# Kernel tuning notes

Hardware: AMD Instinct MI355X
Metric: run time of the kernel (lower is better)

The kernel has to match this reference:

```python
import jax, jax.numpy as jnp
import numpy as np

D_MODEL = 1024
N_HEADS = 16
D_HEAD = 64


def setup_inputs() -> dict:
    key = jax.random.key(0)
    ks = jax.random.split(key, 9)
    B, T = 2, 2048
    s_in = 1.0 / np.sqrt(D_MODEL)
    s_o = 1.0 / np.sqrt(N_HEADS * D_HEAD)
    return {
        "x": jax.random.normal(ks[0], (B, T, D_MODEL), dtype=jnp.float32),
        "wq": jax.random.normal(ks[1], (D_MODEL, N_HEADS * D_HEAD), dtype=jnp.float32) * s_in,
        "bq": jax.random.normal(ks[2], (N_HEADS * D_HEAD,), dtype=jnp.float32) * 0.01,
        "wk": jax.random.normal(ks[3], (D_MODEL, N_HEADS * D_HEAD), dtype=jnp.float32) * s_in,
        "bk": jax.random.normal(ks[4], (N_HEADS * D_HEAD,), dtype=jnp.float32) * 0.01,
        "wv": jax.random.normal(ks[5], (D_MODEL, N_HEADS * D_HEAD), dtype=jnp.float32) * s_in,
        "bv": jax.random.normal(ks[6], (N_HEADS * D_HEAD,), dtype=jnp.float32) * 0.01,
        "wo": jax.random.normal(ks[7], (N_HEADS * D_HEAD, D_MODEL), dtype=jnp.float32) * s_o,
        "bo": jax.random.normal(ks[8], (D_MODEL,), dtype=jnp.float32) * 0.01,
    }


def reference(x, wq, bq, wk, bk, wv, bv, wo, bo):
    B, T, _ = x.shape
    H, Dh = N_HEADS, D_HEAD
    # projections -> [B, H, T, Dh]
    q = (x @ wq + bq).reshape(B, T, H, Dh).transpose(0, 2, 1, 3)
    k = (x @ wk + bk).reshape(B, T, H, Dh).transpose(0, 2, 1, 3)
    v = (x @ wv + bv).reshape(B, T, H, Dh).transpose(0, 2, 1, 3)
    scale = 1.0 / np.sqrt(Dh).astype(np.float32)
    attn = jnp.einsum("bhqd,bhkd->bhqk", q, k) * scale  # [B,H,T,T]
    causal = jnp.tril(jnp.ones((T, T), dtype=bool))
    attn = jnp.where(causal, attn, jnp.float32(-jnp.inf))
    attn = jax.nn.softmax(attn, axis=-1)
    out = jnp.einsum("bhqk,bhkd->bhqd", attn, v)  # [B,H,T,Dh]
    out = out.transpose(0, 2, 1, 3).reshape(B, T, H * Dh)
    return out @ wo + bo
```

## Files before the change

### kernel.cpp

```cpp
#include <hip/hip_runtime.h>
#include <math.h>

#define D_MODEL 1024
#define N_HEADS 16
#define D_HEAD  64
#define B_SZ    2
#define T_SEQ   2048

typedef short bf16x8 __attribute__((ext_vector_type(8)));
typedef short bf16x4 __attribute__((ext_vector_type(4)));
typedef float f32x4  __attribute__((ext_vector_type(4)));
typedef unsigned short us4 __attribute__((ext_vector_type(4)));

__device__ __forceinline__ unsigned short f2bf(float f) {
  union { float f; unsigned u; } v; v.f = f;
  unsigned r = v.u + 0x7FFFu + ((v.u >> 16) & 1u);
  return (unsigned short)(r >> 16);
}
__device__ __forceinline__ float bf2f(unsigned short s) {
  union { unsigned u; float f; } v; v.u = ((unsigned)s) << 16;
  return v.f;
}
__device__ __forceinline__ unsigned pack2_rtz(float lo, float hi) {
  union { float f; unsigned u; } a, b; a.f = hi; b.f = lo;
  return __builtin_amdgcn_perm(a.u, b.u, 0x07060302u);
}

__device__ __forceinline__ void async_copy16(const unsigned short* g, unsigned short* l) {
  __builtin_amdgcn_global_load_lds(
      (__attribute__((address_space(1))) void*)(g),
      (__attribute__((address_space(3))) void*)(l), 16, 0, 0);
}

__device__ __forceinline__ unsigned short* opart_ptr(
    unsigned short* wtd, unsigned short* xbd, int p) {
  const size_t off = (size_t)p * 2048;
  const size_t RA  = (size_t)3 * 1024 * 1024;
  return (off < RA) ? (wtd + off) : (xbd + (off - RA));
}

__global__ __launch_bounds__(256) void conv_all(
    const float* __restrict__ x,
    const float* __restrict__ wq, const float* __restrict__ wk,
    const float* __restrict__ wv, const float* __restrict__ wo,
    unsigned short* __restrict__ wt, unsigned short* __restrict__ xb)
{
  const int z = blockIdx.z;
  if (z < 4) {
    const float* W = (z == 0) ? wq : (z == 1) ? wk : (z == 2) ? wv : wo;
    unsigned short* O = wt + (size_t)z * D_MODEL * D_MODEL;
    __shared__ float t[32][33];
    const int tx = threadIdx.x & 31, ty = threadIdx.x >> 5;
    const int kb = blockIdx.x * 32, nb = blockIdx.y * 32;
    #pragma unroll
    for (int i = 0; i < 4; i++)
      t[ty + i * 8][tx] = W[(size_t)(kb + ty + i * 8) * D_MODEL + nb + tx];
    __syncthreads();
    #pragma unroll
    for (int i = 0; i < 4; i++)
      O[(size_t)(nb + ty + i * 8) * D_MODEL + kb + tx] = f2bf(t[tx][ty + i * 8]);
  } else {
    const int row = (z - 4) * 1024 + blockIdx.y * 32 + (threadIdx.x >> 3);
    const int col = blockIdx.x * 32 + (threadIdx.x & 7) * 4;
    float4 v = *(const float4*)&x[(size_t)row * D_MODEL + col];
    us4 o = { f2bf(v.x), f2bf(v.y), f2bf(v.z), f2bf(v.w) };
    *(us4*)&xb[(size_t)row * D_MODEL + col] = o;
  }
}

#define BKg 64
#define QSCALE 0.180336879f

__global__ __launch_bounds__(256) void qkv_gemm(
    const unsigned short* __restrict__ A, const unsigned short* __restrict__ Bt,
    const float* __restrict__ bq, const float* __restrict__ bk,
    const float* __restrict__ bv, unsigned short* __restrict__ qkv,
    unsigned short* __restrict__ vT)
{
  __shared__ unsigned short As[128 * BKg];
  __shared__ unsigned short Bs[64 * BKg];

  const int tid  = threadIdx.x;
  const int wv   = tid >> 6;
  const int lane = tid & 63;
  const int lr   = lane & 15;
  const int quad = lane >> 4;
  const int wm   = wv >> 1;
  const int wn   = wv & 1;
  const int row0 = blockIdx.x * 128;
  const int col0 = blockIdx.y * 64;
  const int K = D_MODEL;

  const int mid = col0 >> 10;
  const float* bias = (mid == 0) ? bq : (mid == 1) ? bk : bv;

  f32x4 acc[8];
  #pragma unroll
  for (int i = 0; i < 8; i++) acc[i] = (f32x4){0.f, 0.f, 0.f, 0.f};

  for (int k0 = 0; k0 < K; k0 += BKg) {
    #pragma unroll
    for (int it = 0; it < 4; it++) {
      const int gg = wv * 256 + it * 64 + lane;
      const int r  = gg >> 3;
      const int gc = ((gg & 7) ^ (r & 7)) * 8;
      async_copy16(A + (size_t)(row0 + r) * K + k0 + gc,
                   (unsigned short*)As + (size_t)(wv * 256 + it * 64) * 8);
    }
    #pragma unroll
    for (int it = 0; it < 2; it++) {
      const int gg = wv * 128 + it * 64 + lane;
      const int r  = gg >> 3;
      const int gc = ((gg & 7) ^ (r & 7)) * 8;
      async_copy16(Bt + (size_t)(col0 + r) * K + k0 + gc,
                   (unsigned short*)Bs + (size_t)(wv * 128 + it * 64) * 8);
    }
    __syncthreads();

    if (mid == 2) {
      bf16x8 aF[4][2], bF[2][2];
      #pragma unroll
      for (int hf = 0; hf < 2; hf++) {
        const int kc = (hf * 4 + quad) ^ (lr & 7);
        #pragma unroll
        for (int mi = 0; mi < 4; mi++)
          aF[mi][hf] = *(const bf16x8*)&As[(wm * 64 + mi * 16 + lr) * BKg + kc * 8];
        #pragma unroll
        for (int ni = 0; ni < 2; ni++)
          bF[ni][hf] = *(const bf16x8*)&Bs[(wn * 32 + ni * 16 + lr) * BKg + kc * 8];
      }
      #pragma unroll
      for (int hf = 0; hf < 2; hf++)
        #pragma unroll
        for (int mi = 0; mi < 4; mi++)
          #pragma unroll
          for (int ni = 0; ni < 2; ni++)
            acc[mi * 2 + ni] = __builtin_amdgcn_mfma_f32_16x16x32_bf16(
                aF[mi][hf], bF[ni][hf], acc[mi * 2 + ni], 0, 0, 0);
    } else {
      bf16x8 aF[2][2], bF[4][2];
      #pragma unroll
      for (int hf = 0; hf < 2; hf++) {
        const int kc = (hf * 4 + quad) ^ (lr & 7);
        #pragma unroll
        for (int mi = 0; mi < 2; mi++)
          aF[mi][hf] = *(const bf16x8*)&Bs[(wm * 32 + mi * 16 + lr) * BKg + kc * 8];
        #pragma unroll
        for (int ni = 0; ni < 4; ni++)
          bF[ni][hf] = *(const bf16x8*)&As[(wn * 64 + ni * 16 + lr) * BKg + kc * 8];
      }
      #pragma unroll
      for (int hf = 0; hf < 2; hf++)
        #pragma unroll
        for (int mi = 0; mi < 2; mi++)
          #pragma unroll
          for (int ni = 0; ni < 4; ni++)
            acc[mi * 4 + ni] = __builtin_amdgcn_mfma_f32_16x16x32_bf16(
                aF[mi][hf], bF[ni][hf], acc[mi * 4 + ni], 0, 0, 0);
    }
    __syncthreads();
  }

  if (mid == 2) {
    #pragma unroll
    for (int ni = 0; ni < 2; ni++) {
      const int nn = (col0 & 1023) + wn * 32 + ni * 16 + lr;
      const float bv_ = bias[nn];
      const int h = nn >> 6, d = nn & 63;
      #pragma unroll
      for (int mi = 0; mi < 4; mi++) {
        const int t0_ = row0 + wm * 64 + mi * 16 + quad * 4;
        const int b = t0_ >> 11, tl = t0_ & 2047;
        us4 o;
        #pragma unroll
        for (int i = 0; i < 4; i++) o[i] = f2bf(acc[mi * 2 + ni][i] + bv_);
        *(us4*)&vT[((size_t)(b * N_HEADS + h) * D_HEAD + d) * T_SEQ + tl] = o;
      }
    }
  } else {
    unsigned short* dst = qkv + (size_t)mid * (4096u * 1024u);
    const float qs = (mid == 0) ? QSCALE : 1.0f;
    #pragma unroll
    for (int ni = 0; ni < 4; ni++) {
      const int t = row0 + wn * 64 + ni * 16 + lr;
      const int b = t >> 11, tl = t & 2047;
      #pragma unroll
      for (int mi = 0; mi < 2; mi++) {
        const int f = (col0 & 1023) + wm * 32 + mi * 16 + quad * 4;
        const int h = f >> 6, d = f & 63;
        const float4 b4 = *(const float4*)&bias[f];
        us4 o;
        o[0] = f2bf((acc[mi * 4 + ni][0] + b4.x) * qs);
        o[1] = f2bf((acc[mi * 4 + ni][1] + b4.y) * qs);
        o[2] = f2bf((acc[mi * 4 + ni][2] + b4.z) * qs);
        o[3] = f2bf((acc[mi * 4 + ni][3] + b4.w) * qs);
        *(us4*)&dst[((size_t)(b * N_HEADS + h) * T_SEQ + tl) * D_HEAD + d] = o;
      }
    }
  }
}

__global__ __launch_bounds__(256) void mfma_gemm(
    const unsigned short* __restrict__ A, const unsigned short* __restrict__ Bt,
    const float* __restrict__ bias, float* __restrict__ C,
    int M, int N, int K)
{
  __shared__ unsigned short As[128 * BKg];
  __shared__ unsigned short Bs[64 * BKg];

  const int tid  = threadIdx.x;
  const int wv   = tid >> 6;
  const int lane = tid & 63;
  const int lr   = lane & 15;
  const int quad = lane >> 4;
  const int wm   = wv >> 1;
  const int wn   = wv & 1;
  const int row0 = blockIdx.x * 128;
  const int col0 = blockIdx.y * 64;

  f32x4 acc[4][2];
  #pragma unroll
  for (int mi = 0; mi < 4; mi++)
    #pragma unroll
    for (int ni = 0; ni < 2; ni++) acc[mi][ni] = (f32x4){0.f, 0.f, 0.f, 0.f};

  for (int k0 = 0; k0 < K; k0 += BKg) {
    #pragma unroll
    for (int it = 0; it < 4; it++) {
      const int gg = wv * 256 + it * 64 + lane;
      const int r  = gg >> 3;
      const int gc = ((gg & 7) ^ (r & 7)) * 8;
      async_copy16(A + (size_t)(row0 + r) * K + k0 + gc,
                   (unsigned short*)As + (size_t)(wv * 256 + it * 64) * 8);
    }
    #pragma unroll
    for (int it = 0; it < 2; it++) {
      const int gg = wv * 128 + it * 64 + lane;
      const int r  = gg >> 3;
      const int gc = ((gg & 7) ^ (r & 7)) * 8;
      async_copy16(Bt + (size_t)(col0 + r) * K + k0 + gc,
                   (unsigned short*)Bs + (size_t)(wv * 128 + it * 64) * 8);
    }
    __syncthreads();

    bf16x8 aF[4][2], bF[2][2];
    #pragma unroll
    for (int hf = 0; hf < 2; hf++) {
      const int kc = (hf * 4 + quad) ^ (lr & 7);
      #pragma unroll
      for (int mi = 0; mi < 4; mi++)
        aF[mi][hf] = *(const bf16x8*)&As[(wm * 64 + mi * 16 + lr) * BKg + kc * 8];
      #pragma unroll
      for (int ni = 0; ni < 2; ni++)
        bF[ni][hf] = *(const bf16x8*)&Bs[(wn * 32 + ni * 16 + lr) * BKg + kc * 8];
    }
    #pragma unroll
    for (int hf = 0; hf < 2; hf++)
      #pragma unroll
      for (int mi = 0; mi < 4; mi++)
        #pragma unroll
        for (int ni = 0; ni < 2; ni++)
          acc[mi][ni] = __builtin_amdgcn_mfma_f32_16x16x32_bf16(
              aF[mi][hf], bF[ni][hf], acc[mi][ni], 0, 0, 0);
    __syncthreads();
  }

  #pragma unroll
  for (int ni = 0; ni < 2; ni++) {
    const int n = col0 + wn * 32 + ni * 16 + lr;
    const float bv = bias[n];
    #pragma unroll
    for (int mi = 0; mi < 4; mi++) {
      #pragma unroll
      for (int i = 0; i < 4; i++) {
        const int m = row0 + wm * 64 + mi * 16 + quad * 4 + i;
        C[(size_t)m * N + n] = acc[mi][ni][i] + bv;
      }
    }
  }
}

__global__ __launch_bounds__(256) void flash_part(
    const unsigned short* __restrict__ Q, const unsigned short* __restrict__ K,
    const unsigned short* __restrict__ Vt, unsigned short* __restrict__ Out,
    unsigned short* __restrict__ OpA, unsigned short* __restrict__ OpB,
    float* __restrict__ Lpart)
{
  const int bh = blockIdx.x;
  const int y  = blockIdx.y;
  int g, md;
  if (y < 28) { g = 15 - (y >> 1); md = 1 + (y & 1); }
  else        { g = 29 - y; md = 0; }

  const int b  = bh >> 4;
  const int h  = bh & 15;

  const unsigned short* Qb = Q  + (size_t)bh * T_SEQ * D_HEAD;
  const unsigned short* Kb = K  + (size_t)bh * T_SEQ * D_HEAD;
  const unsigned short* Vb = Vt + (size_t)bh * D_HEAD * T_SEQ;

  __shared__ __align__(16) unsigned short Ks[2][64 * 64];
  __shared__ __align__(16) unsigned short Vs[2][64 * 64];

  const int tid  = threadIdx.x;
  const int wv4  = tid >> 6;
  const int lane = tid & 63;
  const int lr   = lane & 15;
  const int quad = lane >> 4;

  const int qg      = 4 * g + wv4;
  const int q0      = qg * 32;
  const int my_full = 2 * g + 1 + (wv4 >> 1);
  const int tstart  = (md == 2) ? (g + 1) : 0;
  const int bend    = (md == 1) ? (g + 1) : (2 * g + 2);
  const int my_end  = (md == 1) ? (g + 1) : my_full;

  const int cbase = (tid & ~63);
  const int rr = tid >> 3;
  const int gcf = ((tid & 7) ^ (rr & 7)) * 8;
  const unsigned short* kp0 = Kb + (size_t)rr * D_HEAD + gcf;
  const unsigned short* vp0 = Vb + (size_t)rr * T_SEQ + gcf;

  auto stage = [&](int buf, int tile) {
    const unsigned short* kt = kp0 + (size_t)tile * (64 * D_HEAD);
    const unsigned short* vt = vp0 + (size_t)tile * 64;
    async_copy16(kt,                    &Ks[buf][(size_t)cbase * 8]);
    async_copy16(kt + 32 * D_HEAD,      &Ks[buf][(size_t)(256 + cbase) * 8]);
    async_copy16(vt,                    &Vs[buf][(size_t)cbase * 8]);
    async_copy16(vt + (size_t)32 * T_SEQ, &Vs[buf][(size_t)(256 + cbase) * 8]);
  };

  bf16x8 bQ[2][2];
  #pragma unroll
  for (int qb = 0; qb < 2; qb++)
    #pragma unroll
    for (int kh = 0; kh < 2; kh++)
      bQ[qb][kh] = *(const bf16x8*)&Qb[(size_t)(q0 + qb * 16 + lr) * D_HEAD + kh * 32 + quad * 8];

  f32x4 oacc[2][4];
  #pragma unroll
  for (int qb = 0; qb < 2; qb++)
    #pragma unroll
    for (int dt = 0; dt < 4; dt++) oacc[qb][dt] = (f32x4){0.f, 0.f, 0.f, 0.f};
  f32x4 lacc[2] = {(f32x4){0.f, 0.f, 0.f, 0.f}, (f32x4){0.f, 0.f, 0.f, 0.f}};

  const bf16x4 vONE = {(short)0x3F80, (short)0x3F80, (short)0x3F80, (short)0x3F80};

  int cur = 0;
  stage(0, tstart);

  for (int j = tstart; j < bend; j++) {
    __syncthreads();
    const bool act = (j < my_end);
    const unsigned short* KsB = &Ks[cur][0];
    const unsigned short* VsB = &Vs[cur][0];
    const int kv0 = j * 64;

    bf16x8 aK[4][2];
    bf16x4 aV[4][4];
    if (act) {
      #pragma unroll
      for (int nt = 0; nt < 4; nt++) {
        const int row = nt * 16 + lr;
        #pragma unroll
        for (int kh = 0; kh < 2; kh++) {
          const int sc = (kh * 4 + quad) ^ (row & 7);
          aK[nt][kh] = *(const bf16x8*)&KsB[row * 64 + sc * 8];
        }
      }
      #pragma unroll
      for (int dt = 0; dt < 4; dt++) {
        const int row = dt * 16 + lr;
        #pragma unroll
        for (int ks = 0; ks < 4; ks++) {
          const int sc = (ks * 2 + (quad >> 1)) ^ (row & 7);
          aV[dt][ks] = *(const bf16x4*)&VsB[row * 64 + sc * 8 + (quad & 1) * 4];
        }
      }
    }

    if (j + 1 < bend) stage(cur ^ 1, j + 1);

    if (act) {
      f32x4 sacc[2][4];
      __builtin_amdgcn_s_setprio(1);
      #pragma unroll
      for (int nt = 0; nt < 4; nt++) {
        #pragma unroll
        for (int qb = 0; qb < 2; qb++) {
          f32x4 c = (f32x4){0.f, 0.f, 0.f, 0.f};
          c = __builtin_amdgcn_mfma_f32_16x16x32_bf16(aK[nt][0], bQ[qb][0], c, 0, 0, 0);
          c = __builtin_amdgcn_mfma_f32_16x16x32_bf16(aK[nt][1], bQ[qb][1], c, 0, 0, 0);
          sacc[qb][nt] = c;
        }
      }
      __builtin_amdgcn_s_setprio(0);

      const bool diag = (j == my_full - 1);
      bf16x4 bP[2][4];
      #pragma unroll
      for (int qb = 0; qb < 2; qb++) {
        if (diag) {
          const int qcol = q0 + qb * 16 + lr;
          #pragma unroll
          for (int nt = 0; nt < 4; nt++)
            #pragma unroll
            for (int i = 0; i < 4; i++)
              if (kv0 + nt * 16 + quad * 4 + i > qcol) sacc[qb][nt][i] = -INFINITY;
        }
        #pragma unroll
        for (int nt = 0; nt < 4; nt++) {
          float p[4];
          #pragma unroll
          for (int i = 0; i < 4; i++)
            p[i] = __builtin_amdgcn_exp2f(sacc[qb][nt][i]);
          union { unsigned u[2]; bf16x4 v; } pk;
          pk.u[0] = pack2_rtz(p[0], p[1]);
          pk.u[1] = pack2_rtz(p[2], p[3]);
          bP[qb][nt] = pk.v;
        }
      }

      __builtin_amdgcn_s_setprio(1);
      #pragma unroll
      for (int ks = 0; ks < 4; ks++) {
        #pragma unroll
        for (int qb = 0; qb < 2; qb++) {
          lacc[qb] = __builtin_amdgcn_mfma_f32_16x16x16bf16_1k(
              vONE, bP[qb][ks], lacc[qb], 0, 0, 0);
          #pragma unroll
          for (int dt = 0; dt < 4; dt++)
            oacc[qb][dt] = __builtin_amdgcn_mfma_f32_16x16x16bf16_1k(
                aV[dt][ks], bP[qb][ks], oacc[qb][dt], 0, 0, 0);
        }
      }
      __builtin_amdgcn_s_setprio(0);
    }
    cur ^= 1;
  }

  float l_i[2] = {lacc[0][0], lacc[1][0]};

  if (md == 0) {
    #pragma unroll
    for (int qb = 0; qb < 2; qb++) {
      const float invl = __builtin_amdgcn_rcpf(l_i[qb]);
      const size_t orow = (size_t)(b * T_SEQ + q0 + qb * 16 + lr) * D_MODEL + h * D_HEAD;
      #pragma unroll
      for (int dt = 0; dt < 4; dt++) {
        us4 o;
        #pragma unroll
        for (int i = 0; i < 4; i++) o[i] = f2bf(oacc[qb][dt][i] * invl);
        *(us4*)&Out[orow + dt * 16 + quad * 4] = o;
      }
    }
  } else {
    const int s = md - 1;
    const int p = (bh * 56 + (qg - 8)) * 2 + s;
    unsigned short* Op = opart_ptr(OpA, OpB, p);
    if (quad == 0) {
      Lpart[(p * 2 + 0) * 16 + lr] = l_i[0];
      Lpart[(p * 2 + 1) * 16 + lr] = l_i[1];
    }
    #pragma unroll
    for (int qb = 0; qb < 2; qb++) {
      #pragma unroll
      for (int dt = 0; dt < 4; dt++) {
        us4 o;
        #pragma unroll
        for (int i = 0; i < 4; i++) o[i] = f2bf(oacc[qb][dt][i]);
        *(us4*)&Op[(size_t)(((qb * 4 + dt) * 64) + lane) * 4] = o;
      }
    }
  }
}

__global__ __launch_bounds__(64) void flash_reduce(
    unsigned short* __restrict__ OpA, unsigned short* __restrict__ OpB,
    const float* __restrict__ Lpart, unsigned short* __restrict__ Out)
{
  const int bh  = blockIdx.x;
  const int qgr = blockIdx.y;
  const int q0  = (8 + qgr) * 32;
  const int b   = bh >> 4;
  const int h   = bh & 15;
  const int lane = threadIdx.x;
  const int lr   = lane & 15;
  const int quad = lane >> 4;

  const int item = bh * 56 + qgr;
  const int p0 = item * 2, p1 = item * 2 + 1;
  const unsigned short* O0 = opart_ptr(OpA, OpB, p0);
  const unsigned short* O1 = opart_ptr(OpA, OpB, p1);

  #pragma unroll
  for (int qb = 0; qb < 2; qb++) {
    const float l0 = Lpart[(p0 * 2 + qb) * 16 + lr];
    const float l1 = Lpart[(p1 * 2 + qb) * 16 + lr];
    const float invL = __builtin_amdgcn_rcpf(l0 + l1);
    const size_t orow = (size_t)(b * T_SEQ + q0 + qb * 16 + lr) * D_MODEL + h * D_HEAD;
    #pragma unroll
    for (int dt = 0; dt < 4; dt++) {
      us4 o0 = *(const us4*)&O0[(size_t)(((qb * 4 + dt) * 64) + lane) * 4];
      us4 o1 = *(const us4*)&O1[(size_t)(((qb * 4 + dt) * 64) + lane) * 4];
      us4 o;
      #pragma unroll
      for (int i = 0; i < 4; i++)
        o[i] = f2bf((bf2f(o0[i]) + bf2f(o1[i])) * invL);
      *(us4*)&Out[orow + dt * 16 + quad * 4] = o;
    }
  }
}

extern "C" void kernel_launch(void* const* d_in, const int* in_sizes, int n_in,
                              void* d_out, int out_size, void* d_ws, size_t ws_size,
                              hipStream_t stream) {
  (void)in_sizes; (void)n_in; (void)out_size; (void)ws_size;

  const float* x  = (const float*)d_in[0];
  const float* wq = (const float*)d_in[1];
  const float* bq = (const float*)d_in[2];
  const float* wk = (const float*)d_in[3];
  const float* bk = (const float*)d_in[4];
  const float* wv = (const float*)d_in[5];
  const float* bv = (const float*)d_in[6];
  const float* wo = (const float*)d_in[7];
  const float* bo = (const float*)d_in[8];
  float* out = (float*)d_out;

  const int M = B_SZ * T_SEQ;
  const int N = D_MODEL;
  const int K = D_MODEL;
  const size_t MN = (size_t)M * N;
  const size_t WN = (size_t)N * N;

  unsigned short* wt    = (unsigned short*)d_ws;
  unsigned short* xb    = wt + 4 * WN;
  unsigned short* qkv   = xb + MN;
  unsigned short* qb    = qkv;
  unsigned short* kb    = qkv + MN;
  unsigned short* vT    = qkv + 2 * MN;
  unsigned short* attnb = vT + MN;
  float* Lpart = (float*)(attnb + MN);

  conv_all<<<dim3(32, 32, 8), dim3(256), 0, stream>>>(x, wq, wk, wv, wo, wt, xb);

  qkv_gemm<<<dim3(M / 128, 48), dim3(256), 0, stream>>>(xb, wt, bq, bk, bv, qkv, vT);

  flash_part<<<dim3(B_SZ * N_HEADS, 30), dim3(256), 0, stream>>>(
      qb, kb, vT, attnb, wt, xb, Lpart);
  flash_reduce<<<dim3(B_SZ * N_HEADS, 56), dim3(64), 0, stream>>>(
      wt, xb, Lpart, attnb);

  mfma_gemm<<<dim3(M / 128, N / 64), dim3(256), 0, stream>>>(attnb, wt + 3 * WN, bo, out, M, N, K);
}
```

Measured before the change: 185.1 us.

## Double-buffer LDS tiles in QKV and output GEMMs to overlap loads with MFMA

Both GEMM kernels now use two LDS buffers per operand. Each iteration loads its fragments from the current buffer, then issues async copies for the next K tile into the other buffer before running the MFMAs. This drops one barrier per iteration and lets global-to-LDS transfers overlap with compute. In exchange it doubles LDS use, which may lower occupancy. Correctness depends on the async copy wait semantics inside the single remaining barrier.

```diff
diff --git a/kernel.cpp b/kernel.cpp
--- a/kernel.cpp
+++ b/kernel.cpp
@@ -69,6 +69,7 @@
 }
 
 #define BKg 64
+#define NTg (D_MODEL / BKg)
 #define QSCALE 0.180336879f
 
 __global__ __launch_bounds__(256) void qkv_gemm(
@@ -77,8 +78,8 @@
     const float* __restrict__ bv, unsigned short* __restrict__ qkv,
     unsigned short* __restrict__ vT)
 {
-  __shared__ unsigned short As[128 * BKg];
-  __shared__ unsigned short Bs[64 * BKg];
+  __shared__ unsigned short As[2][128 * BKg];
+  __shared__ unsigned short Bs[2][64 * BKg];
 
   const int tid  = threadIdx.x;
   const int wv   = tid >> 6;
@@ -98,14 +99,14 @@
   #pragma unroll
   for (int i = 0; i < 8; i++) acc[i] = (f32x4){0.f, 0.f, 0.f, 0.f};
 
-  for (int k0 = 0; k0 < K; k0 += BKg) {
+  auto stage = [&](int buf, int k0) {
     #pragma unroll
     for (int it = 0; it < 4; it++) {
       const int gg = wv * 256 + it * 64 + lane;
       const int r  = gg >> 3;
       const int gc = ((gg & 7) ^ (r & 7)) * 8;
       async_copy16(A + (size_t)(row0 + r) * K + k0 + gc,
-                   (unsigned short*)As + (size_t)(wv * 256 + it * 64) * 8);
+                   &As[buf][(size_t)(wv * 256 + it * 64) * 8]);
     }
     #pragma unroll
     for (int it = 0; it < 2; it++) {
@@ -113,22 +114,44 @@
       const int r  = gg >> 3;
       const int gc = ((gg & 7) ^ (r & 7)) * 8;
       async_copy16(Bt + (size_t)(col0 + r) * K + k0 + gc,
-                   (unsigned short*)Bs + (size_t)(wv * 128 + it * 64) * 8);
-    }
+                   &Bs[buf][(size_t)(wv * 128 + it * 64) * 8]);
+    }
+  };
+
+  int cur = 0;
+  stage(0, 0);
+
+  for (int t = 0; t < NTg; ++t) {
     __syncthreads();
 
+    bf16x8 aF[4][2], bF[4][2];
     if (mid == 2) {
-      bf16x8 aF[4][2], bF[2][2];
       #pragma unroll
       for (int hf = 0; hf < 2; hf++) {
-        const int kc = (hf * 4 + quad) ^ (lr & 7);
+        const int kc = ((hf * 4 + quad) ^ (lr & 7)) * 8;
         #pragma unroll
         for (int mi = 0; mi < 4; mi++)
-          aF[mi][hf] = *(const bf16x8*)&As[(wm * 64 + mi * 16 + lr) * BKg + kc * 8];
+          aF[mi][hf] = *(const bf16x8*)&As[cur][(wm * 64 + mi * 16 + lr) * BKg + kc];
         #pragma unroll
         for (int ni = 0; ni < 2; ni++)
-          bF[ni][hf] = *(const bf16x8*)&Bs[(wn * 32 + ni * 16 + lr) * BKg + kc * 8];
-      }
+          bF[ni][hf] = *(const bf16x8*)&Bs[cur][(wn * 32 + ni * 16 + lr) * BKg + kc];
+      }
+    } else {
+      #pragma unroll
+      for (int hf = 0; hf < 2; hf++) {
+        const int kc = ((hf * 4 + quad) ^ (lr & 7)) * 8;
+        #pragma unroll
+        for (int mi = 0; mi < 2; mi++)
+          aF[mi][hf] = *(const bf16x8*)&Bs[cur][(wm * 32 + mi * 16 + lr) * BKg + kc];
+        #pragma unroll
+        for (int ni = 0; ni < 4; ni++)
+          bF[ni][hf] = *(const bf16x8*)&As[cur][(wn * 64 + ni * 16 + lr) * BKg + kc];
+      }
+    }
+
+    if (t + 1 < NTg) stage(cur ^ 1, (t + 1) * BKg);
+
+    if (mid == 2) {
       #pragma unroll
       for (int hf = 0; hf < 2; hf++)
         #pragma unroll
@@ -138,17 +161,6 @@
             acc[mi * 2 + ni] = __builtin_amdgcn_mfma_f32_16x16x32_bf16(
                 aF[mi][hf], bF[ni][hf], acc[mi * 2 + ni], 0, 0, 0);
     } else {
-      bf16x8 aF[2][2], bF[4][2];
-      #pragma unroll
-      for (int hf = 0; hf < 2; hf++) {
-        const int kc = (hf * 4 + quad) ^ (lr & 7);
-        #pragma unroll
-        for (int mi = 0; mi < 2; mi++)
-          aF[mi][hf] = *(const bf16x8*)&Bs[(wm * 32 + mi * 16 + lr) * BKg + kc * 8];
-        #pragma unroll
-        for (int ni = 0; ni < 4; ni++)
-          bF[ni][hf] = *(const bf16x8*)&As[(wn * 64 + ni * 16 + lr) * BKg + kc * 8];
-      }
       #pragma unroll
       for (int hf = 0; hf < 2; hf++)
         #pragma unroll
@@ -158,7 +170,7 @@
             acc[mi * 4 + ni] = __builtin_amdgcn_mfma_f32_16x16x32_bf16(
                 aF[mi][hf], bF[ni][hf], acc[mi * 4 + ni], 0, 0, 0);
     }
-    __syncthreads();
+    cur ^= 1;
   }
 
   if (mid == 2) {
@@ -205,8 +217,8 @@
     const float* __restrict__ bias, float* __restrict__ C,
     int M, int N, int K)
 {
-  __shared__ unsigned short As[128 * BKg];
-  __shared__ unsigned short Bs[64 * BKg];
+  __shared__ unsigned short As[2][128 * BKg];
+  __shared__ unsigned short Bs[2][64 * BKg];
 
   const int tid  = threadIdx.x;
   const int wv   = tid >> 6;
@@ -224,14 +236,14 @@
     #pragma unroll
     for (int ni = 0; ni < 2; ni++) acc[mi][ni] = (f32x4){0.f, 0.f, 0.f, 0.f};
 
-  for (int k0 = 0; k0 < K; k0 += BKg) {
+  auto stage = [&](int buf, int k0) {
     #pragma unroll
     for (int it = 0; it < 4; it++) {
       const int gg = wv * 256 + it * 64 + lane;
       const int r  = gg >> 3;
       const int gc = ((gg & 7) ^ (r & 7)) * 8;
       async_copy16(A + (size_t)(row0 + r) * K + k0 + gc,
-                   (unsigned short*)As + (size_t)(wv * 256 + it * 64) * 8);
+                   &As[buf][(size_t)(wv * 256 + it * 64) * 8]);
     }
     #pragma unroll
     for (int it = 0; it < 2; it++) {
@@ -239,21 +251,31 @@
       const int r  = gg >> 3;
       const int gc = ((gg & 7) ^ (r & 7)) * 8;
       async_copy16(Bt + (size_t)(col0 + r) * K + k0 + gc,
-                   (unsigned short*)Bs + (size_t)(wv * 128 + it * 64) * 8);
-    }
+                   &Bs[buf][(size_t)(wv * 128 + it * 64) * 8]);
+    }
+  };
+
+  const int NT = K / BKg;
+  int cur = 0;
+  stage(0, 0);
+
+  for (int t = 0; t < NT; ++t) {
     __syncthreads();
 
     bf16x8 aF[4][2], bF[2][2];
     #pragma unroll
     for (int hf = 0; hf < 2; hf++) {
-      const int kc = (hf * 4 + quad) ^ (lr & 7);
+      const int kc = ((hf * 4 + quad) ^ (lr & 7)) * 8;
       #pragma unroll
       for (int mi = 0; mi < 4; mi++)
-        aF[mi][hf] = *(const bf16x8*)&As[(wm * 64 + mi * 16 + lr) * BKg + kc * 8];
+        aF[mi][hf] = *(const bf16x8*)&As[cur][(wm * 64 + mi * 16 + lr) * BKg + kc];
       #pragma unroll
       for (int ni = 0; ni < 2; ni++)
-        bF[ni][hf] = *(const bf16x8*)&Bs[(wn * 32 + ni * 16 + lr) * BKg + kc * 8];
-    }
+        bF[ni][hf] = *(const bf16x8*)&Bs[cur][(wn * 32 + ni * 16 + lr) * BKg + kc];
+    }
+
+    if (t + 1 < NT) stage(cur ^ 1, (t + 1) * BKg);
+
     #pragma unroll
     for (int hf = 0; hf < 2; hf++)
       #pragma unroll
@@ -262,7 +284,7 @@
         for (int ni = 0; ni < 2; ni++)
           acc[mi][ni] = __builtin_amdgcn_mfma_f32_16x16x32_bf16(
               aF[mi][hf], bF[ni][hf], acc[mi][ni], 0, 0, 0);
-    __syncthreads();
+    cur ^= 1;
   }
 
   #pragma unroll
```

After: 183.8 us. Within noise of the previous version (-0.7%).
